# Kernel tuning notes

Hardware: AMD Instinct MI355X
Metric: run time of the kernel (lower is better)

The kernel has to match this reference:

```python
import jax, jax.numpy as jnp
import numpy as np

SCALES = (4, 2, 2)  # config.latent_structure.scaling_factors


def expand_length(x, scale):
    # Faithful to conv_transpose1d with an all-ones (D, D, scale) kernel at
    # stride=scale: out[b, l*scale + j, d] = sum_d' x[b, l, d'] for all j, d.
    # i.e. channel-sum broadcast to all channels, repeated `scale` times in L.
    s = jnp.sum(x, axis=-1, keepdims=True)            # [B, L, 1]
    y = jnp.broadcast_to(s, x.shape)                  # [B, L, D]
    return jnp.repeat(y, scale, axis=1)               # [B, L*scale, D]


def setup_inputs() -> dict:
    key = jax.random.key(0)
    k0, k1, k2, k3 = jax.random.split(key, 4)
    B, L, D0 = 8, 64, 256
    D1, D2, D3 = 512, 768, 768
    scale = 0.02
    return {
        "z_1": jax.random.normal(k0, (B, L, D0), jnp.float32),
        "W1": jax.random.normal(k1, (D0, D1), jnp.float32) * scale,
        "b1": jnp.zeros((D1,), jnp.float32),
        "W2": jax.random.normal(k2, (D1, D2), jnp.float32) * scale,
        "b2": jnp.zeros((D2,), jnp.float32),
        "W3": jax.random.normal(k3, (D2, D3), jnp.float32) * scale,
        "b3": jnp.zeros((D3,), jnp.float32),
    }


def reference(z_1, W1, b1, W2, b2, W3, b3):
    x = z_1
    for s in SCALES:                 # scaled_inputs is None -> plain loop
        x = expand_length(x, s)
    x = jnp.einsum("bld,de->ble", x, W1) + b1   # embedding_upscale1
    x = expand_length(x, SCALES[1])
    x = jnp.einsum("bld,de->ble", x, W2) + b2   # embedding_upscale2
    x = expand_length(x, SCALES[2])
    x = jnp.einsum("bld,de->ble", x, W3) + b3   # embedding_upscale3
    return x  # [8, 4096, 768]
```

## Files before the change

kernel.cpp:

```cpp
#include <hip/hip_runtime.h>

typedef float f4 __attribute__((ext_vector_type(4)));

#define NF_W1P  0
#define NF_W2P  32
#define NF_B1   128
#define NF_B2   129
#define NF_S0   130
#define NF_CW3P 656
#define NF_CW3  6800
#define NF_U    7568

__device__ __forceinline__ float wave_reduce(float v) {
#pragma unroll
    for (int off = 32; off; off >>= 1) v += __shfl_down(v, off, 64);
    return v;
}

__device__ __forceinline__ float block_reduce_256(float v) {
    __shared__ float sm[4];
    v = wave_reduce(v);
    int lane = threadIdx.x & 63, wid = threadIdx.x >> 6;
    if (lane == 0) sm[wid] = v;
    __syncthreads();
    if (threadIdx.x == 0) v = sm[0] + sm[1] + sm[2] + sm[3];
    return v;
}

__global__ __launch_bounds__(256) void k_reduce(
    const float* __restrict__ z1, const float* __restrict__ W1,
    const float* __restrict__ b1, const float* __restrict__ W2,
    const float* __restrict__ b2, const float* __restrict__ W3,
    float* __restrict__ f) {
    const int blk = blockIdx.x, tid = threadIdx.x;
    if (blk < 128) {
        const float* p = (blk < 32) ? (W1 + blk * 4096) : (W2 + (blk - 32) * 4096);
        float s = 0.f;
#pragma unroll
        for (int i = 0; i < 16; ++i) s += p[tid + i * 256];
        s = block_reduce_256(s);
        if (tid == 0) f[blk] = s;
    } else if (blk == 128) {
        float s = b1[tid] + b1[tid + 256];
        s = block_reduce_256(s);
        if (tid == 0) f[NF_B1] = s;
    } else if (blk == 129) {
        float s = b2[tid] + b2[tid + 256] + b2[tid + 512];
        s = block_reduce_256(s);
        if (tid == 0) f[NF_B2] = s;
    } else if (blk < 258) {
        const int lane = tid & 63, wid = tid >> 6;
        const int row = (blk - 130) * 4 + wid;
        const float* p = z1 + row * 256;
        float s = p[lane] + p[lane + 64] + p[lane + 128] + p[lane + 192];
        s = wave_reduce(s);
        if (lane == 0) f[NF_S0 + row] = s;
    } else {
        const int g = blk - 258;
        const int cg = g % 3, rg = g / 3;
        const int e = cg * 256 + tid;
        const float* p = W3 + rg * 96 * 768 + e;
        float s = 0.f;
#pragma unroll 8
        for (int d = 0; d < 96; ++d) s += p[d * 768];
        f[NF_CW3P + rg * 768 + e] = s;
    }
}

__global__ __launch_bounds__(768) void k_combine(float* __restrict__ f) {
    __shared__ float s12_sm[2];
    const int tid = threadIdx.x;
    float c = 0.f;
#pragma unroll
    for (int r = 0; r < 8; ++r) c += f[NF_CW3P + r * 768 + tid];
    f[NF_CW3 + tid] = c;
    if (tid < 64) {
        float a = (tid < 32) ? f[NF_W1P + tid] : 0.f;
        float b = f[NF_W2P + tid] + ((tid < 32) ? f[NF_W2P + 64 + tid] : 0.f);
#pragma unroll
        for (int off = 32; off; off >>= 1) {
            a += __shfl_down(a, off, 64);
            b += __shfl_down(b, off, 64);
        }
        if (tid == 0) { s12_sm[0] = a; s12_sm[1] = b; }
    }
    __syncthreads();
    if (tid < 512) {
        const float S1 = s12_sm[0], S2 = s12_sm[1];
        f[NF_U + tid] = (65536.0f * f[NF_S0 + tid] * S1 + f[NF_B1]) * S2 + f[NF_B2];
    }
}

__global__ __launch_bounds__(256) void k_write(
    const float* __restrict__ f, const float* __restrict__ b3,
    float* __restrict__ out) {
    const int tid = threadIdx.x;
    const int lane = tid & 63, wid = tid >> 6;
    const float u = f[NF_U + (blockIdx.x >> 2)];
    const f4* __restrict__ cw4 = (const f4*)(f + NF_CW3);
    const f4* __restrict__ b4  = (const f4*)b3;
    f4 v[3];
#pragma unroll
    for (int k = 0; k < 3; ++k) {
        const int e4 = lane + k * 64;
        const f4 c = cw4[e4];
        const f4 b = b4[e4];
        v[k].x = fmaf(u, c.x, b.x);
        v[k].y = fmaf(u, c.y, b.y);
        v[k].z = fmaf(u, c.z, b.z);
        v[k].w = fmaf(u, c.w, b.w);
    }
#pragma unroll
    for (int r = 0; r < 4; ++r) {
        const int row = blockIdx.x * 16 + wid * 4 + r;
        f4* o = (f4*)(out + (size_t)row * 768);
#pragma unroll
        for (int k = 0; k < 3; ++k)
            __builtin_nontemporal_store(v[k], &o[lane + k * 64]);
    }
}

extern "C" void kernel_launch(void* const* d_in, const int* in_sizes, int n_in,
                              void* d_out, int out_size, void* d_ws, size_t ws_size,
                              hipStream_t stream) {
    const float* z1 = (const float*)d_in[0];
    const float* W1 = (const float*)d_in[1];
    const float* b1 = (const float*)d_in[2];
    const float* W2 = (const float*)d_in[3];
    const float* b2 = (const float*)d_in[4];
    const float* W3 = (const float*)d_in[5];
    const float* b3 = (const float*)d_in[6];
    float* out = (float*)d_out;
    float* f = (float*)d_ws;

    k_reduce<<<282, 256, 0, stream>>>(z1, W1, b1, W2, b2, W3, f);
    k_combine<<<1, 768, 0, stream>>>(f);
    k_write<<<2048, 256, 0, stream>>>(f, b3, out);
}
```

Baseline: 29.40 us.

## Eliminate combine kernel by folding its work into reduce and write kernels

Removes the single-block k_combine launch. The W3 column sums are now finished inside k_reduce through a shared-memory reduction over 8 row groups, with each block owning 32 columns. Each k_write block recomputes the S1/S2 scalars and u from the partial sums. The scalar reductions in k_reduce are also vectorised with float4 loads. This cuts one kernel launch and its serial dependency, at the price of redundant small reductions in every write block and an extra __syncthreads.

```diff
diff --git a/kernel.cpp b/kernel.cpp
--- a/kernel.cpp
+++ b/kernel.cpp
@@ -7,9 +7,7 @@
 #define NF_B1   128
 #define NF_B2   129
 #define NF_S0   130
-#define NF_CW3P 656
-#define NF_CW3  6800
-#define NF_U    7568
+#define NF_CW3  656
 
 __device__ __forceinline__ float wave_reduce(float v) {
 #pragma unroll
@@ -34,60 +32,43 @@
     float* __restrict__ f) {
     const int blk = blockIdx.x, tid = threadIdx.x;
     if (blk < 128) {
-        const float* p = (blk < 32) ? (W1 + blk * 4096) : (W2 + (blk - 32) * 4096);
-        float s = 0.f;
-#pragma unroll
-        for (int i = 0; i < 16; ++i) s += p[tid + i * 256];
-        s = block_reduce_256(s);
+        const f4* p = (blk < 32) ? (const f4*)(W1 + blk * 4096)
+                                 : (const f4*)(W2 + (blk - 32) * 4096);
+        f4 a = p[tid] + p[tid + 256] + p[tid + 512] + p[tid + 768];
+        float s = block_reduce_256(a.x + a.y + a.z + a.w);
         if (tid == 0) f[blk] = s;
     } else if (blk == 128) {
-        float s = b1[tid] + b1[tid + 256];
+        float s = 0.f;
+        if (tid < 128) { f4 a = ((const f4*)b1)[tid]; s = a.x + a.y + a.z + a.w; }
         s = block_reduce_256(s);
         if (tid == 0) f[NF_B1] = s;
     } else if (blk == 129) {
-        float s = b2[tid] + b2[tid + 256] + b2[tid + 512];
+        float s = 0.f;
+        if (tid < 192) { f4 a = ((const f4*)b2)[tid]; s = a.x + a.y + a.z + a.w; }
         s = block_reduce_256(s);
         if (tid == 0) f[NF_B2] = s;
     } else if (blk < 258) {
         const int lane = tid & 63, wid = tid >> 6;
         const int row = (blk - 130) * 4 + wid;
-        const float* p = z1 + row * 256;
-        float s = p[lane] + p[lane + 64] + p[lane + 128] + p[lane + 192];
-        s = wave_reduce(s);
+        f4 a = ((const f4*)(z1 + row * 256))[lane];
+        float s = wave_reduce(a.x + a.y + a.z + a.w);
         if (lane == 0) f[NF_S0 + row] = s;
     } else {
         const int g = blk - 258;
-        const int cg = g % 3, rg = g / 3;
-        const int e = cg * 256 + tid;
-        const float* p = W3 + rg * 96 * 768 + e;
+        const int c = tid & 31, rg = tid >> 5;
+        const float* p = W3 + (rg * 96) * 768 + g * 32 + c;
         float s = 0.f;
 #pragma unroll 8
-        for (int d = 0; d < 96; ++d) s += p[d * 768];
-        f[NF_CW3P + rg * 768 + e] = s;
-    }
-}
-
-__global__ __launch_bounds__(768) void k_combine(float* __restrict__ f) {
-    __shared__ float s12_sm[2];
-    const int tid = threadIdx.x;
-    float c = 0.f;
+        for (int i = 0; i < 96; ++i) s += p[i * 768];
+        __shared__ float sm[8][32];
+        sm[rg][c] = s;
+        __syncthreads();
+        if (tid < 32) {
+            float acc = 0.f;
 #pragma unroll
-    for (int r = 0; r < 8; ++r) c += f[NF_CW3P + r * 768 + tid];
-    f[NF_CW3 + tid] = c;
-    if (tid < 64) {
-        float a = (tid < 32) ? f[NF_W1P + tid] : 0.f;
-        float b = f[NF_W2P + tid] + ((tid < 32) ? f[NF_W2P + 64 + tid] : 0.f);
-#pragma unroll
-        for (int off = 32; off; off >>= 1) {
-            a += __shfl_down(a, off, 64);
-            b += __shfl_down(b, off, 64);
+            for (int r = 0; r < 8; ++r) acc += sm[r][tid];
+            f[NF_CW3 + g * 32 + tid] = acc;
         }
-        if (tid == 0) { s12_sm[0] = a; s12_sm[1] = b; }
-    }
-    __syncthreads();
-    if (tid < 512) {
-        const float S1 = s12_sm[0], S2 = s12_sm[1];
-        f[NF_U + tid] = (65536.0f * f[NF_S0 + tid] * S1 + f[NF_B1]) * S2 + f[NF_B2];
     }
 }
 
@@ -96,19 +77,40 @@
     float* __restrict__ out) {
     const int tid = threadIdx.x;
     const int lane = tid & 63, wid = tid >> 6;
-    const float u = f[NF_U + (blockIdx.x >> 2)];
+
     const f4* __restrict__ cw4 = (const f4*)(f + NF_CW3);
     const f4* __restrict__ b4  = (const f4*)b3;
+    f4 c[3], b[3];
+#pragma unroll
+    for (int k = 0; k < 3; ++k) {
+        c[k] = cw4[lane + k * 64];
+        b[k] = b4[lane + k * 64];
+    }
+
+    __shared__ float u_sm;
+    if (tid < 64) {
+        float a = (lane < 32) ? f[NF_W1P + lane] : 0.f;
+        float w = f[NF_W2P + lane] + ((lane < 32) ? f[NF_W2P + 64 + lane] : 0.f);
+#pragma unroll
+        for (int off = 32; off; off >>= 1) {
+            a += __shfl_down(a, off, 64);
+            w += __shfl_down(w, off, 64);
+        }
+        if (lane == 0) {
+            const float s0v = f[NF_S0 + (blockIdx.x >> 2)];
+            u_sm = (65536.0f * s0v * a + f[NF_B1]) * w + f[NF_B2];
+        }
+    }
+    __syncthreads();
+    const float u = u_sm;
+
     f4 v[3];
 #pragma unroll
     for (int k = 0; k < 3; ++k) {
-        const int e4 = lane + k * 64;
-        const f4 c = cw4[e4];
-        const f4 b = b4[e4];
-        v[k].x = fmaf(u, c.x, b.x);
-        v[k].y = fmaf(u, c.y, b.y);
-        v[k].z = fmaf(u, c.z, b.z);
-        v[k].w = fmaf(u, c.w, b.w);
+        v[k].x = fmaf(u, c[k].x, b[k].x);
+        v[k].y = fmaf(u, c[k].y, b[k].y);
+        v[k].z = fmaf(u, c[k].z, b[k].z);
+        v[k].w = fmaf(u, c[k].w, b[k].w);
     }
 #pragma unroll
     for (int r = 0; r < 4; ++r) {
@@ -134,6 +136,5 @@
     float* f = (float*)d_ws;
 
     k_reduce<<<282, 256, 0, stream>>>(z1, W1, b1, W2, b2, W3, f);
-    k_combine<<<1, 768, 0, stream>>>(f);
     k_write<<<2048, 256, 0, stream>>>(f, b3, out);
 }
```

After: 28.04 us. 1.05x faster.
